# Kernel tuning notes

Hardware: AMD Instinct MI355X
Metric: run time of the kernel (lower is better)

The kernel has to match this reference:

```python
import jax, jax.numpy as jnp
import numpy as np

HID = 50

def _lstm_cell(x_t, h, c, W_ih, W_hh, b_ih, b_hh):
    # PyTorch LSTMCell gate order: i, f, g, o
    gates = x_t @ W_ih.T + b_ih + h @ W_hh.T + b_hh  # [B, 4*HID]
    i, f, g, o = jnp.split(gates, 4, axis=-1)
    i = jax.nn.sigmoid(i)
    f = jax.nn.sigmoid(f)
    g = jnp.tanh(g)
    o = jax.nn.sigmoid(o)
    c = f * c + i * g
    h = o * jnp.tanh(c)
    return h, c


def setup_inputs() -> dict:
    key = jax.random.key(0)
    ks = jax.random.split(key, 8)
    B, T = 2048, 512
    stdv = 1.0 / np.sqrt(HID)
    x = jax.random.normal(ks[0], (B, T), dtype=jnp.float32)
    W_ih = jax.random.uniform(ks[1], (4 * HID, 1), jnp.float32, -stdv, stdv)
    W_hh = jax.random.uniform(ks[2], (4 * HID, HID), jnp.float32, -stdv, stdv)
    b_ih = jax.random.uniform(ks[3], (4 * HID,), jnp.float32, -stdv, stdv)
    b_hh = jax.random.uniform(ks[4], (4 * HID,), jnp.float32, -stdv, stdv)
    W_out = jax.random.uniform(ks[5], (1, HID), jnp.float32, -stdv, stdv)
    b_out = jax.random.uniform(ks[6], (1,), jnp.float32, -stdv, stdv)
    return {"x": x, "W_ih": W_ih, "W_hh": W_hh, "b_ih": b_ih,
            "b_hh": b_hh, "W_out": W_out, "b_out": b_out, "future": 64}


def reference(x, W_ih, W_hh, b_ih, b_hh, W_out, b_out, future):
    B, T = x.shape
    h0 = jnp.zeros((B, HID), dtype=x.dtype)
    c0 = jnp.zeros((B, HID), dtype=x.dtype)
    xs = x.T[:, :, None]  # [T, B, 1]

    def seq_step(carry, x_t):
        h, c = carry
        h, c = _lstm_cell(x_t, h, c, W_ih, W_hh, b_ih, b_hh)
        out = h @ W_out.T + b_out  # [B, 1]
        return (h, c), out

    (h, c), outs = jax.lax.scan(seq_step, (h0, c0), xs)  # outs: [T, B, 1]

    def fut_step(carry, _):
        h, c, out = carry
        h, c = _lstm_cell(out, h, c, W_ih, W_hh, b_ih, b_hh)
        out = h @ W_out.T + b_out
        return (h, c, out), out

    _, fut_outs = jax.lax.scan(fut_step, (h, c, outs[-1]), None, length=future)
    all_outs = jnp.concatenate([outs, fut_outs], axis=0)  # [T+future, B, 1]
    return jnp.transpose(all_outs[:, :, 0])  # [B, T+future]
```

## Files before the change

kernel.cpp:

```cpp
#include <hip/hip_runtime.h>

typedef float v2f __attribute__((ext_vector_type(2)));
typedef float v4f __attribute__((ext_vector_type(4)));

#define BATCH 2048
#define TSEQ 512
#define FUT 64
#define TOUT (TSEQ + FUT)
#define HID 50


__device__ __forceinline__ float rcp_f(float x) { return __builtin_amdgcn_rcpf(x); }
__device__ __forceinline__ float sigm(float x)  { return rcp_f(1.f + __expf(-x)); }
__device__ __forceinline__ float tanh_f(float x){ return 1.f - 2.f * rcp_f(__expf(2.f * x) + 1.f); }

__device__ __forceinline__ void pkfma(v2f& acc, v2f a, v2f b) {
  asm("v_pk_fma_f32 %0, %1, %2, %0" : "+v"(acc) : "v"(a), "v"(b));
}

__global__ __launch_bounds__(128, 3) void lstm_seq_kernel(
    const float* __restrict__ x,
    const float* __restrict__ W_ih,
    const float* __restrict__ W_hh,
    const float* __restrict__ b_ih,
    const float* __restrict__ b_hh,
    const float* __restrict__ W_out,
    const float* __restrict__ b_out,
    float* __restrict__ out)
{
  __shared__ float sH[64];
  __shared__ v2f   sGb[HID];
  __shared__ float sOut[1];
  __shared__ float sx[TSEQ];

  const int tid  = threadIdx.x;
  const int wv   = tid >> 6;
  const int lane = tid & 63;
  const int row  = blockIdx.x;

  for (int i = tid; i < TSEQ; i += 128) sx[i] = x[row * TSEQ + i];
  if (tid < 64) sH[tid] = 0.f;

  const bool act = (lane < HID);
  const int  kk  = act ? lane : 0;
  const int  rA  = (2 * wv) * HID + kk;
  const int  rB  = (2 * wv + 1) * HID + kk;

  v2f wA[25], wB[25];
  {
    const v2f* pA = (const v2f*)(W_hh + rA * HID);
    const v2f* pB = (const v2f*)(W_hh + rB * HID);
    #pragma unroll
    for (int j = 0; j < 25; ++j) { wA[j] = pA[j]; wB[j] = pB[j]; }
  }
  const float bA  = b_ih[rA] + b_hh[rA];
  const float bB  = b_ih[rB] + b_hh[rB];
  const float wxA = W_ih[rA];
  const float wxB = W_ih[rB];
  const float wout = act ? W_out[kk] : 0.f;
  const float bout = b_out[0];

  float c = 0.f;
  float* orow = out + (size_t)row * TOUT;
  const v4f* sH4 = (const v4f*)sH;
  const v2f* sH2 = (const v2f*)sH;

  __syncthreads();

  #pragma unroll 1
  for (int t = 0; t < TOUT; ++t) {
    const float xv = (t < TSEQ) ? sx[t] : sOut[0];

    v2f aA = {fmaf(xv, wxA, bA), 0.f};
    v2f aB = {fmaf(xv, wxB, bB), 0.f};
    #pragma unroll
    for (int q = 0; q < 12; ++q) {
      v4f h4 = sH4[q];
      v2f ha = {h4.x, h4.y}, hb = {h4.z, h4.w};
      pkfma(aA, wA[2 * q], ha); pkfma(aA, wA[2 * q + 1], hb);
      pkfma(aB, wB[2 * q], ha); pkfma(aB, wB[2 * q + 1], hb);
    }
    { v2f ht = sH2[24]; pkfma(aA, wA[24], ht); pkfma(aB, wB[24], ht); }
    const float pa = aA.x + aA.y;
    const float pb = aB.x + aB.y;

    v2f gp;
    if (wv == 0) gp = (v2f){sigm(pa),  sigm(pb)};
    else         gp = (v2f){tanh_f(pa), sigm(pb)};
    if (wv == 1 && act) sGb[kk] = gp;
    __syncthreads();

    if (wv == 0) {
      const v2f go = sGb[kk];
      c = fmaf(gp.y, c, gp.x * go.x);
      const float h = act ? go.y * tanh_f(c) : 0.f;
      sH[lane] = h;
      float p = h * wout;
      p += __shfl_xor(p, 1);
      p += __shfl_xor(p, 2);
      p += __shfl_xor(p, 4);
      p += __shfl_xor(p, 8);
      p += __shfl_xor(p, 16);
      p += __shfl_xor(p, 32);
      const float ot = p + bout;
      if (lane == 0) { orow[t] = ot; sOut[0] = ot; }
    }
    __syncthreads();
  }
}

extern "C" void kernel_launch(void* const* d_in, const int* in_sizes, int n_in,
                              void* d_out, int out_size, void* d_ws, size_t ws_size,
                              hipStream_t stream) {
  const float* x     = (const float*)d_in[0];
  const float* W_ih  = (const float*)d_in[1];
  const float* W_hh  = (const float*)d_in[2];
  const float* b_ih  = (const float*)d_in[3];
  const float* b_hh  = (const float*)d_in[4];
  const float* W_out = (const float*)d_in[5];
  const float* b_out = (const float*)d_in[6];
  float* out = (float*)d_out;

  lstm_seq_kernel<<<BATCH, 128, 0, stream>>>(
      x, W_ih, W_hh, b_ih, b_hh, W_out, b_out, out);
}
```

Before: 603.2 us.

## Split LSTM gates across four waves, one gate row per thread

Each block now runs 256 threads, four wavefronts, with each wave computing one gate (i, f, g, o) for its 50 hidden units. Before, two waves each computed two gate rows. This halves the per-thread matvec work and register footprint, and uses two independent accumulators to shorten the FMA dependency chain. All waves now read the four gates from shared memory and redundantly compute the cell update. The loop is also split into the sequence phase and the feedback phase to remove a per-step branch. The cost is twice the threads per block and more shared-memory traffic per step, while the two barriers per step remain.

New measurement: 908.6 us. 50.6% more time.

```diff
diff --git a/kernel.cpp b/kernel.cpp
--- a/kernel.cpp
+++ b/kernel.cpp
@@ -18,7 +18,7 @@
   asm("v_pk_fma_f32 %0, %1, %2, %0" : "+v"(acc) : "v"(a), "v"(b));
 }
 
-__global__ __launch_bounds__(128, 3) void lstm_seq_kernel(
+__global__ __launch_bounds__(256, 4) void lstm_seq_kernel(
     const float* __restrict__ x,
     const float* __restrict__ W_ih,
     const float* __restrict__ W_hh,
@@ -29,7 +29,7 @@
     float* __restrict__ out)
 {
   __shared__ float sH[64];
-  __shared__ v2f   sGb[HID];
+  __shared__ float sG[4][64];
   __shared__ float sOut[1];
   __shared__ float sx[TSEQ];
 
@@ -38,25 +38,21 @@
   const int lane = tid & 63;
   const int row  = blockIdx.x;
 
-  for (int i = tid; i < TSEQ; i += 128) sx[i] = x[row * TSEQ + i];
+  for (int i = tid; i < TSEQ; i += 256) sx[i] = x[row * TSEQ + i];
   if (tid < 64) sH[tid] = 0.f;
 
   const bool act = (lane < HID);
   const int  kk  = act ? lane : 0;
-  const int  rA  = (2 * wv) * HID + kk;
-  const int  rB  = (2 * wv + 1) * HID + kk;
+  const int  r   = wv * HID + kk;
 
-  v2f wA[25], wB[25];
+  v2f w[25];
   {
-    const v2f* pA = (const v2f*)(W_hh + rA * HID);
-    const v2f* pB = (const v2f*)(W_hh + rB * HID);
+    const v2f* p = (const v2f*)(W_hh + r * HID);
     #pragma unroll
-    for (int j = 0; j < 25; ++j) { wA[j] = pA[j]; wB[j] = pB[j]; }
+    for (int j = 0; j < 25; ++j) w[j] = p[j];
   }
-  const float bA  = b_ih[rA] + b_hh[rA];
-  const float bB  = b_ih[rB] + b_hh[rB];
-  const float wxA = W_ih[rA];
-  const float wxB = W_ih[rB];
+  const float bg0 = b_ih[r] + b_hh[r];
+  const float wx  = W_ih[r];
   const float wout = act ? W_out[kk] : 0.f;
   const float bout = b_out[0];
 
@@ -67,33 +63,36 @@
 
   __syncthreads();
 
-  #pragma unroll 1
-  for (int t = 0; t < TOUT; ++t) {
-    const float xv = (t < TSEQ) ? sx[t] : sOut[0];
-
-    v2f aA = {fmaf(xv, wxA, bA), 0.f};
-    v2f aB = {fmaf(xv, wxB, bB), 0.f};
+  auto step = [&](float xv, int t) {
+    v2f a2 = {fmaf(xv, wx, bg0), 0.f};
+    v2f a2b = {0.f, 0.f};
     #pragma unroll
-    for (int q = 0; q < 12; ++q) {
+    for (int q = 0; q < 6; ++q) {
       v4f h4 = sH4[q];
       v2f ha = {h4.x, h4.y}, hb = {h4.z, h4.w};
-      pkfma(aA, wA[2 * q], ha); pkfma(aA, wA[2 * q + 1], hb);
-      pkfma(aB, wB[2 * q], ha); pkfma(aB, wB[2 * q + 1], hb);
+      pkfma(a2,  w[2 * q],     ha);
+      pkfma(a2b, w[2 * q + 1], hb);
     }
-    { v2f ht = sH2[24]; pkfma(aA, wA[24], ht); pkfma(aB, wB[24], ht); }
-    const float pa = aA.x + aA.y;
-    const float pb = aB.x + aB.y;
-
-    v2f gp;
-    if (wv == 0) gp = (v2f){sigm(pa),  sigm(pb)};
-    else         gp = (v2f){tanh_f(pa), sigm(pb)};
-    if (wv == 1 && act) sGb[kk] = gp;
+    #pragma unroll
+    for (int q = 6; q < 12; ++q) {
+      v4f h4 = sH4[q];
+      v2f ha = {h4.x, h4.y}, hb = {h4.z, h4.w};
+      pkfma(a2,  w[2 * q],     ha);
+      pkfma(a2b, w[2 * q + 1], hb);
+    }
+    { v2f ht = sH2[24]; pkfma(a2, w[24], ht); }
+    const float pre = (a2.x + a2b.x) + (a2.y + a2b.y);
+    const float g   = (wv == 2) ? tanh_f(pre) : sigm(pre);
+    sG[wv][lane] = g;
     __syncthreads();
 
+    const float gi = sG[0][lane];
+    const float gf = sG[1][lane];
+    const float gg = sG[2][lane];
+    const float go = sG[3][lane];
+    c = fmaf(gf, c, gi * gg);
+    const float h = act ? go * tanh_f(c) : 0.f;
     if (wv == 0) {
-      const v2f go = sGb[kk];
-      c = fmaf(gp.y, c, gp.x * go.x);
-      const float h = act ? go.y * tanh_f(c) : 0.f;
       sH[lane] = h;
       float p = h * wout;
       p += __shfl_xor(p, 1);
@@ -106,7 +105,12 @@
       if (lane == 0) { orow[t] = ot; sOut[0] = ot; }
     }
     __syncthreads();
-  }
+  };
+
+  #pragma unroll 1
+  for (int t = 0; t < TSEQ; ++t) step(sx[t], t);
+  #pragma unroll 1
+  for (int t = TSEQ; t < TOUT; ++t) step(sOut[0], t);
 }
 
 extern "C" void kernel_launch(void* const* d_in, const int* in_sizes, int n_in,
@@ -121,6 +125,6 @@
   const float* b_out = (const float*)d_in[6];
   float* out = (float*)d_out;
 
-  lstm_seq_kernel<<<BATCH, 128, 0, stream>>>(
+  lstm_seq_kernel<<<BATCH, 256, 0, stream>>>(
       x, W_ih, W_hh, b_ih, b_hh, W_out, b_out, out);
 }
```
